# Kernel optimization log

Hardware: AMD Instinct MI355X
Metric: run time of the kernel (lower is better)

The kernel has to match this reference:

```python
import jax, jax.numpy as jnp
import numpy as np

V = 50257
D = 512
T = 1024


def setup_inputs() -> dict:
    key = jax.random.key(0)
    ks = jax.random.split(key, 12)
    si = (2.0 / (V + D)) ** 0.5   # xavier-ish scale for input matrices
    sh = (1.0 / D) ** 0.5         # scale for recurrent matrices
    so = (2.0 / (V + D)) ** 0.5
    return {
        "idx": jax.random.randint(ks[0], (T,), 0, V, dtype=jnp.int32),
        "W_ii": jax.random.normal(ks[1], (D, V), jnp.float32) * si,
        "W_if": jax.random.normal(ks[2], (D, V), jnp.float32) * si,
        "W_io": jax.random.normal(ks[3], (D, V), jnp.float32) * si,
        "W_ig": jax.random.normal(ks[4], (D, V), jnp.float32) * si,
        "W_hi": jax.random.normal(ks[5], (D, D), jnp.float32) * sh,
        "W_hf": jax.random.normal(ks[6], (D, D), jnp.float32) * sh,
        "W_ho": jax.random.normal(ks[7], (D, D), jnp.float32) * sh,
        "W_hg": jax.random.normal(ks[8], (D, D), jnp.float32) * sh,
        "b_i": jnp.zeros((D,), jnp.float32),
        "b_f": jnp.ones((D,), jnp.float32),
        "b_o": jnp.zeros((D,), jnp.float32),
        "b_g": jnp.zeros((D,), jnp.float32),
        "W_out": jax.random.normal(ks[9], (V, D), jnp.float32) * so,
        "b_out": jnp.zeros((V,), jnp.float32),
    }


def reference(idx, W_ii, W_if, W_io, W_ig, W_hi, W_hf, W_ho, W_hg,
              b_i, b_f, b_o, b_g, W_out, b_out):
    # One-hot @ W.T == column gather: W[:, tok]. Dropout is identity (eval mode).
    dims = W_hi.shape[0]

    def step(carry, tok):
        h, c = carry
        i = jax.nn.sigmoid(W_ii[:, tok] + b_i + W_hi @ h)
        f = jax.nn.sigmoid(W_if[:, tok] + b_f + W_hf @ h)
        o = jax.nn.sigmoid(W_io[:, tok] + b_o + W_ho @ h)
        g = jnp.tanh(W_ig[:, tok] + b_g + W_hg @ h)
        c_new = f * c + i * g
        h_new = o * jnp.tanh(c_new)
        logits = W_out @ h_new + b_out          # [V]
        return (h_new, c_new), jax.nn.log_softmax(logits)

    h0 = jnp.zeros((dims,), W_hi.dtype)
    c0 = jnp.zeros((dims,), W_hi.dtype)
    (h, c), log_probs = jax.lax.scan(step, (h0, c0), idx)
    return log_probs, h, c  # log_probs: [T, V]
```

## Files before the change

kernel.cpp:

```cpp
#include <hip/hip_runtime.h>
#include <hip/hip_bf16.h>

#define VV 50257
#define DD 512
#define TT 1024
#define NBLK 197
#define PSTR 200
#define NBR 64
#define GEMB (NBLK*8)
#define TOTB (NBR + GEMB)

typedef __bf16 bf16;
typedef __attribute__((ext_vector_type(8))) __bf16 bf16x8;
typedef __attribute__((ext_vector_type(4))) float f32x4;
typedef __attribute__((ext_vector_type(4))) unsigned int u32x4;

__global__ __launch_bounds__(512) __attribute__((amdgpu_waves_per_eu(2, 2)))
void mega_kernel(
    const int* __restrict__ idx,
    const float* __restrict__ Wii, const float* __restrict__ Wif,
    const float* __restrict__ Wio, const float* __restrict__ Wig,
    const float* __restrict__ Whi, const float* __restrict__ Whf,
    const float* __restrict__ Who, const float* __restrict__ Whg,
    const float* __restrict__ bi, const float* __restrict__ bfv,
    const float* __restrict__ bo, const float* __restrict__ bg,
    const float* __restrict__ Wout, const float* __restrict__ bout,
    unsigned long long* __restrict__ Hpack,
    float* __restrict__ Cout, float* __restrict__ Pmax, float* __restrict__ Psum,
    float* __restrict__ out_tail) {
  __shared__ char smem[55296];
  const int tid = threadIdx.x;

  if (blockIdx.x < NBR) {
    float (*hsh)[DD] = (float(*)[DD])smem;
    int* idxs = (int*)(smem + 4096);
    const int b = blockIdx.x;

    idxs[tid] = idx[tid];
    idxs[tid + 512] = idx[tid + 512];

    const int lane = tid & 63, w = tid >> 6;
    const int hd = (b << 3) + w;

    f32x4 wr0[4], wr1[4];
    #pragma unroll
    for (int gg = 0; gg < 4; ++gg) {
      const float* Wg = (gg == 0) ? Whi : (gg == 1) ? Whf : (gg == 2) ? Who : Whg;
      wr0[gg] = *(const f32x4*)&Wg[(size_t)hd*DD + (lane << 2)];
      wr1[gg] = *(const f32x4*)&Wg[(size_t)hd*DD + 256 + (lane << 2)];
    }
    #pragma unroll
    for (int gg = 0; gg < 4; ++gg) {
      asm volatile("" : "+v"(wr0[gg]));
      asm volatile("" : "+v"(wr1[gg]));
    }

    const float* wxp = nullptr;
    float bias = 0.f;
    if (lane < 4) {
      const float* Wx = (lane == 0) ? Wii : (lane == 1) ? Wif : (lane == 2) ? Wio : Wig;
      const float* bx = (lane == 0) ? bi : (lane == 1) ? bfv : (lane == 2) ? bo : bg;
      wxp = &Wx[(size_t)hd * VV];
      bias = bx[hd];
    }
    float c = 0.f, hout = 0.f;
    __syncthreads();

    for (int t = 0; t < TT; ++t) {
      float xv = 0.f;
      if (lane < 4) xv = wxp[idxs[t]] + bias;

      float* hb = hsh[t & 1];
      if (t > 0) {
        const unsigned long long* src = &Hpack[(size_t)(t-1)*DD + tid];
        unsigned long long v;
        do {
          asm volatile("global_load_dwordx2 %0, %1, off sc1\n\t"
                       "s_waitcnt vmcnt(0)"
                       : "=v"(v) : "v"(src) : "memory");
        } while (__builtin_expect((unsigned)(v >> 32) != (unsigned)t, 0));
        hb[tid] = __uint_as_float((unsigned)v);
      } else {
        hb[tid] = 0.f;
      }
      __syncthreads();

      const f32x4 h0 = *(const f32x4*)&hb[lane << 2];
      const f32x4 h1 = *(const f32x4*)&hb[256 + (lane << 2)];
      f32x4 m0 = wr0[0]*h0 + wr1[0]*h1;
      f32x4 m1 = wr0[1]*h0 + wr1[1]*h1;
      f32x4 m2 = wr0[2]*h0 + wr1[2]*h1;
      f32x4 m3 = wr0[3]*h0 + wr1[3]*h1;
      float a0 = m0[0]+m0[1]+m0[2]+m0[3];
      float a1 = m1[0]+m1[1]+m1[2]+m1[3];
      float a2 = m2[0]+m2[1]+m2[2]+m2[3];
      float a3 = m3[0]+m3[1]+m3[2]+m3[3];
      #pragma unroll
      for (int mask = 1; mask < 64; mask <<= 1) {
        a0 += __shfl_xor(a0, mask);
        a1 += __shfl_xor(a1, mask);
        a2 += __shfl_xor(a2, mask);
        a3 += __shfl_xor(a3, mask);
      }

      float myacc = (lane == 0) ? a0 : (lane == 1) ? a1 : (lane == 2) ? a2 : a3;
      float pre = myacc + xv;
      bool isg = (lane == 3);
      float e1 = __expf(isg ? -2.f * pre : -pre);
      float rr = 1.f / (1.f + e1);
      float act = isg ? (2.f * rr - 1.f) : rr;

      float ia = __shfl(act, 0);
      float fa = __shfl(act, 1);
      float oa = __shfl(act, 2);
      float ga = __shfl(act, 3);

      if (lane == 0) {
        c = fa * c + ia * ga;
        float e2 = __expf(-2.f * c);
        float th = 2.f / (1.f + e2) - 1.f;
        hout = oa * th;
        unsigned long long pk =
            ((unsigned long long)(unsigned)(t + 1) << 32) |
            (unsigned long long)__float_as_uint(hout);
        __hip_atomic_store(&Hpack[(size_t)t*DD + hd], pk, __ATOMIC_RELAXED,
                           __HIP_MEMORY_SCOPE_AGENT);
        if (t == TT - 1) { out_tail[hd] = hout; out_tail[DD + hd] = c; }
      }
    }
    return;
  }

  bf16* As = (bf16*)smem;
  bf16* Bs = (bf16*)(smem + 8192);
  float (*Cs)[16][72] = (float(*)[16][72])smem;
  float* partm = (float*)(smem + 36864);
  float* parts = (float*)(smem + 37376);

  const int gb = blockIdx.x - NBR;
  const int my = gb / NBLK;
  const int nb = gb % NBLK;
  const int m0 = my << 7, n0 = nb << 8;
  const int w = tid >> 6, l = tid & 63;
  const int wr = w >> 2, wc = w & 3;

  if (tid == 0) {
    const unsigned long long* gp =
        &Hpack[(size_t)(m0 + 127)*DD + ((unsigned)(nb*67 + my*13) & 511)];
    for (;;) {
      unsigned long long v = __hip_atomic_load(gp, __ATOMIC_RELAXED,
                                               __HIP_MEMORY_SCOPE_AGENT);
      if ((unsigned)(v >> 32) == (unsigned)(m0 + 128)) break;
      __builtin_amdgcn_s_sleep(32);
    }
  }
  __syncthreads();

  const int ar = tid >> 2;
  const int ac = (tid & 3) << 3;
  const unsigned expst = (unsigned)(m0 + ar + 1);
  const unsigned long long* apb = &Hpack[(size_t)(m0 + ar)*DD + ac];
  const int br = tid >> 1;
  const int bc = (tid & 1) << 4;
  const bool bok = (n0 + br) < VV;
  const float* bpb = &Wout[(size_t)(n0 + br)*DD + bc];

  f32x4 acc[4][4] = {};

  for (int k0 = 0; k0 < DD; k0 += 32) {
    u32x4 a0, a1, a2, a3;
    const unsigned long long* ap = apb + k0;
    for (;;) {
      asm volatile("global_load_dwordx4 %0, %4, off sc1\n\t"
                   "global_load_dwordx4 %1, %4, off offset:16 sc1\n\t"
                   "global_load_dwordx4 %2, %4, off offset:32 sc1\n\t"
                   "global_load_dwordx4 %3, %4, off offset:48 sc1\n\t"
                   "s_waitcnt vmcnt(0)"
                   : "=&v"(a0), "=&v"(a1), "=&v"(a2), "=&v"(a3)
                   : "v"(ap) : "memory");
      __builtin_amdgcn_sched_barrier(0);
      if (a0[1] == expst && a0[3] == expst && a1[1] == expst && a1[3] == expst &&
          a2[1] == expst && a2[3] == expst && a3[1] == expst && a3[3] == expst)
        break;
      __builtin_amdgcn_s_sleep(1);
    }
    bf16x8 av;
    av[0] = (bf16)__uint_as_float(a0[0]); av[1] = (bf16)__uint_as_float(a0[2]);
    av[2] = (bf16)__uint_as_float(a1[0]); av[3] = (bf16)__uint_as_float(a1[2]);
    av[4] = (bf16)__uint_as_float(a2[0]); av[5] = (bf16)__uint_as_float(a2[2]);
    av[6] = (bf16)__uint_as_float(a3[0]); av[7] = (bf16)__uint_as_float(a3[2]);
    *(bf16x8*)&As[ar*32 + ac] = av;

    bf16x8 bv0, bv1;
    if (bok) {
      const float* bp = bpb + k0;
      f32x4 b0 = *(const f32x4*)bp;
      f32x4 b1 = *(const f32x4*)(bp + 4);
      f32x4 b2 = *(const f32x4*)(bp + 8);
      f32x4 b3 = *(const f32x4*)(bp + 12);
      bv0[0]=(bf16)b0[0]; bv0[1]=(bf16)b0[1]; bv0[2]=(bf16)b0[2]; bv0[3]=(bf16)b0[3];
      bv0[4]=(bf16)b1[0]; bv0[5]=(bf16)b1[1]; bv0[6]=(bf16)b1[2]; bv0[7]=(bf16)b1[3];
      bv1[0]=(bf16)b2[0]; bv1[1]=(bf16)b2[1]; bv1[2]=(bf16)b2[2]; bv1[3]=(bf16)b2[3];
      bv1[4]=(bf16)b3[0]; bv1[5]=(bf16)b3[1]; bv1[6]=(bf16)b3[2]; bv1[7]=(bf16)b3[3];
    } else {
      #pragma unroll
      for (int e = 0; e < 8; ++e) { bv0[e] = (bf16)0.f; bv1[e] = (bf16)0.f; }
    }
    *(bf16x8*)&Bs[br*32 + bc] = bv0;
    *(bf16x8*)&Bs[br*32 + bc + 8] = bv1;

    __syncthreads();
    bf16x8 af[4], bfr[4];
    #pragma unroll
    for (int mi = 0; mi < 4; ++mi)
      af[mi] = *(const bf16x8*)&As[(wr*64 + mi*16 + (l & 15))*32 + (l >> 4)*8];
    #pragma unroll
    for (int ni = 0; ni < 4; ++ni)
      bfr[ni] = *(const bf16x8*)&Bs[(wc*64 + ni*16 + (l & 15))*32 + (l >> 4)*8];
    #pragma unroll
    for (int mi = 0; mi < 4; ++mi)
      #pragma unroll
      for (int ni = 0; ni < 4; ++ni)
        acc[mi][ni] = __builtin_amdgcn_mfma_f32_16x16x32_bf16(af[mi], bfr[ni], acc[mi][ni], 0, 0, 0);
    __syncthreads();
  }

  float bbv[4];
  bool colok[4];
  #pragma unroll
  for (int ni = 0; ni < 4; ++ni) {
    int col = n0 + wc*64 + ni*16 + (l & 15);
    colok[ni] = (col < VV);
    bbv[ni] = colok[ni] ? bout[col] : 0.f;
  }

  #pragma unroll
  for (int mi = 0; mi < 4; ++mi) {
    #pragma unroll
    for (int ni = 0; ni < 4; ++ni)
      #pragma unroll
      for (int r = 0; r < 4; ++r)
        Cs[w][(l >> 4)*4 + r][ni*16 + (l & 15)] = acc[mi][ni][r] + bbv[ni];

    #pragma unroll
    for (int r = 0; r < 4; ++r) {
      float v0 = colok[0] ? acc[mi][0][r] + bbv[0] : -1e30f;
      float v1 = colok[1] ? acc[mi][1][r] + bbv[1] : -1e30f;
      float v2 = colok[2] ? acc[mi][2][r] + bbv[2] : -1e30f;
      float v3 = colok[3] ? acc[mi][3][r] + bbv[3] : -1e30f;
      float pm = fmaxf(fmaxf(v0, v1), fmaxf(v2, v3));
      #pragma unroll
      for (int mk = 1; mk < 16; mk <<= 1) pm = fmaxf(pm, __shfl_xor(pm, mk));
      float ps = __expf(v0 - pm) + __expf(v1 - pm) + __expf(v2 - pm) + __expf(v3 - pm);
      #pragma unroll
      for (int mk = 1; mk < 16; mk <<= 1) ps += __shfl_xor(ps, mk);
      if ((l & 15) == 0) {
        partm[(wr*4 + wc)*16 + (l >> 4)*4 + r] = pm;
        parts[(wr*4 + wc)*16 + (l >> 4)*4 + r] = ps;
      }
    }
    __syncthreads();
    if (tid < 32) {
      int wr2 = tid >> 4, row16 = tid & 15;
      float M = -1e30f, S = 0.f;
      #pragma unroll
      for (int q = 0; q < 4; ++q) {
        float mm = partm[(wr2*4 + q)*16 + row16];
        float sp = parts[(wr2*4 + q)*16 + row16];
        float nm = fmaxf(M, mm);
        S = S*__expf(M - nm) + sp*__expf(mm - nm);
        M = nm;
      }
      int gr = m0 + wr2*64 + mi*16 + row16;
      Pmax[(size_t)gr*PSTR + nb] = M;
      Psum[(size_t)gr*PSTR + nb] = S;
    }

    const int rbase = m0 + wr*64 + mi*16;
    #pragma unroll
    for (int i = 0; i < 4; ++i) {
      int idx2 = i*64 + l;
      int row = idx2 >> 4, quad = idx2 & 15;
      int col = n0 + wc*64 + quad*4;
      f32x4 v = *(const f32x4*)&Cs[w][row][quad*4];
      float* dst = &Cout[(size_t)(rbase + row)*VV + col];
      if (col + 3 < VV) {
        asm volatile("global_store_dwordx4 %0, %1, off"
                     :: "v"(dst), "v"(v) : "memory");
      } else {
        #pragma unroll
        for (int e = 0; e < 4; ++e)
          if (col + e < VV) dst[e] = v[e];
      }
    }
    __syncthreads();
  }
}

__global__ __launch_bounds__(512) void lsm_kernel(float* __restrict__ logits,
                                                  const float* __restrict__ Pmax,
                                                  const float* __restrict__ Psum) {
  const int t = blockIdx.x, tid = threadIdx.x;
  float* row = logits + (size_t)t*VV;

  float m = -1e30f, s = 0.f;
  if (tid < NBLK) {
    m = Pmax[(size_t)t*PSTR + tid];
    s = Psum[(size_t)t*PSTR + tid];
  }
  #pragma unroll
  for (int mask = 1; mask < 64; mask <<= 1) {
    float om = __shfl_xor(m, mask);
    float os = __shfl_xor(s, mask);
    float nm = fmaxf(m, om);
    s = s*__expf(m - nm) + os*__expf(om - nm);
    m = nm;
  }
  __shared__ float sm[8], ss[8], lse_sh;
  int wv = tid >> 6;
  if ((tid & 63) == 0) { sm[wv] = m; ss[wv] = s; }
  __syncthreads();
  if (tid == 0) {
    float M = sm[0], S = ss[0];
    for (int i2 = 1; i2 < 8; ++i2) {
      float nm = fmaxf(M, sm[i2]);
      S = S*__expf(M - nm) + ss[i2]*__expf(sm[i2] - nm);
      M = nm;
    }
    lse_sh = M + logf(S);
  }
  __syncthreads();
  const float lse = lse_sh;

  const size_t base = (size_t)t * VV;
  const int head = (int)((4 - (base & 3)) & 3);
  const int nvec = (VV - head) >> 2;
  const int tail0 = head + (nvec << 2);
  if (tid < head) row[tid] -= lse;
  else if (tid >= 508 && (tail0 + (tid - 508)) < VV) row[tail0 + (tid - 508)] -= lse;
  for (int i = tid; i < nvec; i += 512) {
    float* p = &row[head + (i << 2)];
    f32x4 x = *(const f32x4*)p;
    x[0] -= lse; x[1] -= lse; x[2] -= lse; x[3] -= lse;
    *(f32x4*)p = x;
  }
}

extern "C" void kernel_launch(void* const* d_in, const int* in_sizes, int n_in,
                              void* d_out, int out_size, void* d_ws, size_t ws_size,
                              hipStream_t stream) {
  const int*   idx  = (const int*)d_in[0];
  const float* Wii  = (const float*)d_in[1];
  const float* Wif  = (const float*)d_in[2];
  const float* Wio  = (const float*)d_in[3];
  const float* Wig  = (const float*)d_in[4];
  const float* Whi  = (const float*)d_in[5];
  const float* Whf  = (const float*)d_in[6];
  const float* Who  = (const float*)d_in[7];
  const float* Whg  = (const float*)d_in[8];
  const float* bi   = (const float*)d_in[9];
  const float* bfv  = (const float*)d_in[10];
  const float* bo   = (const float*)d_in[11];
  const float* bg   = (const float*)d_in[12];
  const float* Wout = (const float*)d_in[13];
  const float* bout = (const float*)d_in[14];
  float* out = (float*)d_out;

  char* ws = (char*)d_ws;
  unsigned long long* Hpack = (unsigned long long*)ws;
  float* Pmax = (float*)(ws + 4194304);
  float* Psum = (float*)(ws + 5013504);

  hipMemsetAsync(Hpack, 0, (size_t)TT*DD*8, stream);
  mega_kernel<<<TOTB, 512, 0, stream>>>(
      idx, Wii, Wif, Wio, Wig, Whi, Whf, Who, Whg, bi, bfv, bo, bg, Wout, bout,
      Hpack, out, Pmax, Psum, out + (size_t)TT*VV);
  lsm_kernel<<<TT, 512, 0, stream>>>(out, Pmax, Psum);
}
```

Baseline: 1.950 ms.

## Fuse log-softmax normalization into persistent kernel via per-row-block completion counters

Removes the separate log-softmax kernel and appends 1024 extra blocks to the mega kernel. Each extra block spins on an atomic counter until all GEMM column blocks for its 128-timestep row block have finished, then subtracts the logsumexp from its row. GEMM blocks increment the counter with release semantics when done. The aim is to overlap the normalization pass with the remaining recurrence and GEMM work and to drop a kernel launch boundary. The risk is that spinning blocks occupy CU slots, and the design relies on block dispatch order to avoid deadlock.

```diff
diff --git a/kernel.cpp b/kernel.cpp
--- a/kernel.cpp
+++ b/kernel.cpp
@@ -8,7 +8,7 @@
 #define PSTR 200
 #define NBR 64
 #define GEMB (NBLK*8)
-#define TOTB (NBR + GEMB)
+#define TOTB (NBR + GEMB + TT)
 
 typedef __bf16 bf16;
 typedef __attribute__((ext_vector_type(8))) __bf16 bf16x8;
@@ -27,7 +27,7 @@
     const float* __restrict__ Wout, const float* __restrict__ bout,
     unsigned long long* __restrict__ Hpack,
     float* __restrict__ Cout, float* __restrict__ Pmax, float* __restrict__ Psum,
-    float* __restrict__ out_tail) {
+    int* __restrict__ donecnt, float* __restrict__ out_tail) {
   __shared__ char smem[55296];
   const int tid = threadIdx.x;
 
@@ -127,6 +127,63 @@
                            __HIP_MEMORY_SCOPE_AGENT);
         if (t == TT - 1) { out_tail[hd] = hout; out_tail[DD + hd] = c; }
       }
+    }
+    return;
+  }
+
+  if (blockIdx.x >= NBR + GEMB) {
+    const int t = blockIdx.x - (NBR + GEMB);
+    float* row = Cout + (size_t)t*VV;
+    float* sm = (float*)smem;
+    float* ss = (float*)(smem + 32);
+    float* lse_p = (float*)(smem + 64);
+
+    if (tid == 0) {
+      while (__hip_atomic_load(&donecnt[t >> 7], __ATOMIC_ACQUIRE,
+                               __HIP_MEMORY_SCOPE_AGENT) != NBLK)
+        __builtin_amdgcn_s_sleep(32);
+    }
+    __syncthreads();
+
+    float m = -1e30f, s = 0.f;
+    if (tid < NBLK) {
+      m = Pmax[(size_t)t*PSTR + tid];
+      s = Psum[(size_t)t*PSTR + tid];
+    }
+    #pragma unroll
+    for (int mask = 1; mask < 64; mask <<= 1) {
+      float om = __shfl_xor(m, mask);
+      float os = __shfl_xor(s, mask);
+      float nm = fmaxf(m, om);
+      s = s*__expf(m - nm) + os*__expf(om - nm);
+      m = nm;
+    }
+    int wv = tid >> 6;
+    if ((tid & 63) == 0) { sm[wv] = m; ss[wv] = s; }
+    __syncthreads();
+    if (tid == 0) {
+      float M = sm[0], S = ss[0];
+      for (int i2 = 1; i2 < 8; ++i2) {
+        float nm = fmaxf(M, sm[i2]);
+        S = S*__expf(M - nm) + ss[i2]*__expf(sm[i2] - nm);
+        M = nm;
+      }
+      *lse_p = M + logf(S);
+    }
+    __syncthreads();
+    const float lse = *lse_p;
+
+    const size_t base = (size_t)t * VV;
+    const int head = (int)((4 - (base & 3)) & 3);
+    const int nvec = (VV - head) >> 2;
+    const int tail0 = head + (nvec << 2);
+    if (tid < head) row[tid] -= lse;
+    else if (tid >= 508 && (tail0 + (tid - 508)) < VV) row[tail0 + (tid - 508)] -= lse;
+    for (int i = tid; i < nvec; i += 512) {
+      float* p = &row[head + (i << 2)];
+      f32x4 x = *(const f32x4*)p;
+      x[0] -= lse; x[1] -= lse; x[2] -= lse; x[3] -= lse;
+      *(f32x4*)p = x;
     }
     return;
   }
@@ -295,55 +352,9 @@
     }
     __syncthreads();
   }
-}
-
-__global__ __launch_bounds__(512) void lsm_kernel(float* __restrict__ logits,
-                                                  const float* __restrict__ Pmax,
-                                                  const float* __restrict__ Psum) {
-  const int t = blockIdx.x, tid = threadIdx.x;
-  float* row = logits + (size_t)t*VV;
-
-  float m = -1e30f, s = 0.f;
-  if (tid < NBLK) {
-    m = Pmax[(size_t)t*PSTR + tid];
-    s = Psum[(size_t)t*PSTR + tid];
-  }
-  #pragma unroll
-  for (int mask = 1; mask < 64; mask <<= 1) {
-    float om = __shfl_xor(m, mask);
-    float os = __shfl_xor(s, mask);
-    float nm = fmaxf(m, om);
-    s = s*__expf(m - nm) + os*__expf(om - nm);
-    m = nm;
-  }
-  __shared__ float sm[8], ss[8], lse_sh;
-  int wv = tid >> 6;
-  if ((tid & 63) == 0) { sm[wv] = m; ss[wv] = s; }
-  __syncthreads();
-  if (tid == 0) {
-    float M = sm[0], S = ss[0];
-    for (int i2 = 1; i2 < 8; ++i2) {
-      float nm = fmaxf(M, sm[i2]);
-      S = S*__expf(M - nm) + ss[i2]*__expf(sm[i2] - nm);
-      M = nm;
-    }
-    lse_sh = M + logf(S);
-  }
-  __syncthreads();
-  const float lse = lse_sh;
-
-  const size_t base = (size_t)t * VV;
-  const int head = (int)((4 - (base & 3)) & 3);
-  const int nvec = (VV - head) >> 2;
-  const int tail0 = head + (nvec << 2);
-  if (tid < head) row[tid] -= lse;
-  else if (tid >= 508 && (tail0 + (tid - 508)) < VV) row[tail0 + (tid - 508)] -= lse;
-  for (int i = tid; i < nvec; i += 512) {
-    float* p = &row[head + (i << 2)];
-    f32x4 x = *(const f32x4*)p;
-    x[0] -= lse; x[1] -= lse; x[2] -= lse; x[3] -= lse;
-    *(f32x4*)p = x;
-  }
+
+  if (tid == 0)
+    __hip_atomic_fetch_add(&donecnt[my], 1, __ATOMIC_RELEASE, __HIP_MEMORY_SCOPE_AGENT);
 }
 
 extern "C" void kernel_launch(void* const* d_in, const int* in_sizes, int n_in,
@@ -370,10 +381,11 @@
   unsigned long long* Hpack = (unsigned long long*)ws;
   float* Pmax = (float*)(ws + 4194304);
   float* Psum = (float*)(ws + 5013504);
+  int*   donecnt = (int*)(ws + 5832704);
 
   hipMemsetAsync(Hpack, 0, (size_t)TT*DD*8, stream);
+  hipMemsetAsync(donecnt, 0, 32, stream);
   mega_kernel<<<TOTB, 512, 0, stream>>>(
       idx, Wii, Wif, Wio, Wig, Whi, Whf, Who, Whg, bi, bfv, bo, bg, Wout, bout,
-      Hpack, out, Pmax, Psum, out + (size_t)TT*VV);
-  lsm_kernel<<<TT, 512, 0, stream>>>(out, Pmax, Psum);
+      Hpack, out, Pmax, Psum, donecnt, out + (size_t)TT*VV);
 }
```

New measurement: 2.008 ms. +3.0%, slower.
